# Optimization experiments

Measured on AMD Instinct MI355X. Metric: run time of the kernel, lower is better.

Reference implementation:

```python
import jax, jax.numpy as jnp
import numpy as np
import math

C = 512
D = C // 4  # 128
SCALE = math.sqrt(D)

def setup_inputs() -> dict:
    key = jax.random.key(0)
    k1, k2, k3, k4 = jax.random.split(key, 4)
    x = jax.random.normal(k1, (8, C, 2048), dtype=jnp.float32)
    # q_conv and k_conv share the same weight (tied in the torch module)
    wqk = jax.random.normal(k2, (D, C), dtype=jnp.float32) * (1.0 / math.sqrt(C))
    wv = jax.random.normal(k3, (D, C), dtype=jnp.float32) * (1.0 / math.sqrt(C))
    bv = jax.random.normal(k4, (D,), dtype=jnp.float32) * 0.01
    return {"x": x, "wqk": wqk, "wv": wv, "bv": bv}

def reference(x, wqk, wv, bv):
    # x: [B, C, N]; 1x1 conv == matmul over channel dim
    xq = jnp.einsum('dc,bcn->bnd', wqk, x)          # [B, N, D]
    xk = jnp.einsum('dc,bcn->bdn', wqk, x)          # [B, D, N]
    xv = jnp.einsum('dc,bcn->bdn', wv, x) + bv[None, :, None]  # [B, D, N]
    energy = jnp.einsum('bnd,bdm->bnm', xq, xk) / SCALE  # [B, N, N]
    attention = jax.nn.softmax(energy, axis=-1)
    x_r = jnp.einsum('bdn,bnm->bdm', xv, attention)  # [B, D, N]
    return x_r
```

## Files before the change

### kernel.cpp

```cpp
#include <hip/hip_runtime.h>

typedef short short4v __attribute__((ext_vector_type(4)));
typedef short short8 __attribute__((ext_vector_type(8)));
typedef float floatx4 __attribute__((ext_vector_type(4)));
typedef unsigned int uint;
typedef unsigned short ushort;

#define CH 512
#define NN 2048
#define DD 128
#define RSCALE 0.08838834764831845f

__device__ __forceinline__ float bf2f(ushort u) {
    union { uint i; float f; } v; v.i = ((uint)u) << 16; return v.f;
}
__device__ __forceinline__ ushort f2bf(float f) {
    union { float f; uint u; } v; v.f = f;
    uint u = v.u;
    return (ushort)((u + 0x7fffu + ((u >> 16) & 1u)) >> 16);
}

__global__ __launch_bounds__(256) void k0_prep(
    const float* __restrict__ wqk, const float* __restrict__ wv,
    ushort* __restrict__ Wbf, float* __restrict__ lsum)
{
    int gid = blockIdx.x * 256 + threadIdx.x;
    int base = gid * 4;
    const float* src = (base < 65536) ? (wqk + base) : (wv + base - 65536);
    float4 v = *(const float4*)src;
    short4v o;
    o[0] = (short)f2bf(v.x); o[1] = (short)f2bf(v.y);
    o[2] = (short)f2bf(v.z); o[3] = (short)f2bf(v.w);
    *(short4v*)&Wbf[base] = o;
    if (gid < 16384) lsum[gid] = 0.0f;
}

__global__ __launch_bounds__(256) void k1_proj(
    const float* __restrict__ x,
    const ushort* __restrict__ Wbf,
    const float* __restrict__ bv,
    ushort* __restrict__ Q,
    ushort* __restrict__ VT)
{
    const int nt = blockIdx.x;
    const int b  = blockIdx.y;
    const int n0 = nt * 32;
    const int t = threadIdx.x;
    const int lane = t & 63, w = t >> 6, l15 = lane & 15, quad = lane >> 4;

    __shared__ __attribute__((aligned(16))) ushort As[32 * 40];
    __shared__ __attribute__((aligned(16))) ushort Bs[256 * 40];
    __shared__ __attribute__((aligned(16))) ushort Vt[128 * 40];

    floatx4 acc[2][4];
#pragma unroll
    for (int i = 0; i < 2; i++)
#pragma unroll
        for (int j = 0; j < 4; j++) acc[i][j] = (floatx4)(0.0f);

    const float* xb = x + b * (CH * NN) + n0;

    for (int c0 = 0; c0 < CH; c0 += 32) {
        {
            int n = t & 31, g = t >> 5;
            short4v v;
#pragma unroll
            for (int i = 0; i < 4; i++)
                v[i] = (short)f2bf(xb[(c0 + g * 4 + i) * NN + n]);
            *(short4v*)&As[n * 40 + g * 4] = v;
        }
#pragma unroll
        for (int rep = 0; rep < 4; rep++) {
            int idx = rep * 256 + t;
            int row = idx >> 2, g = idx & 3;
            *(short8*)&Bs[row * 40 + g * 8] = *(const short8*)&Wbf[row * CH + c0 + g * 8];
        }
        __syncthreads();
        short8 a0 = *(short8*)&As[(l15) * 40 + quad * 8];
        short8 a1 = *(short8*)&As[(16 + l15) * 40 + quad * 8];
#pragma unroll
        for (int dt2 = 0; dt2 < 4; dt2++) {
            short8 bf = *(short8*)&Bs[(w * 64 + dt2 * 16 + l15) * 40 + quad * 8];
            acc[0][dt2] = __builtin_amdgcn_mfma_f32_16x16x32_bf16(a0, bf, acc[0][dt2], 0, 0, 0);
            acc[1][dt2] = __builtin_amdgcn_mfma_f32_16x16x32_bf16(a1, bf, acc[1][dt2], 0, 0, 0);
        }
        __syncthreads();
    }

#pragma unroll
    for (int ns = 0; ns < 2; ns++)
#pragma unroll
        for (int dt2 = 0; dt2 < 4; dt2++) {
            int ds_ = w * 64 + dt2 * 16 + l15;
#pragma unroll
            for (int r = 0; r < 4; r++) {
                int nl = ns * 16 + quad * 4 + r;
                float val = acc[ns][dt2][r];
                if (ds_ < 128) {
                    Q[b * (NN * DD) + (n0 + nl) * DD + ds_] = f2bf(val);
                } else {
                    int dv = ds_ - 128;
                    Vt[dv * 40 + nl] = f2bf(val + bv[dv]);
                }
            }
        }
    __syncthreads();
#pragma unroll
    for (int rep = 0; rep < 2; rep++) {
        int idx = rep * 256 + t;
        int dv = idx >> 2, seg = idx & 3;
        *(short8*)&VT[((size_t)b * DD + dv) * NN + n0 + seg * 8] =
            *(short8*)&Vt[dv * 40 + seg * 8];
    }
}

__global__ __launch_bounds__(256) void kl_sum(
    const ushort* __restrict__ Q,
    float* __restrict__ lsum)
{
    int pid = blockIdx.x;
    const int b = blockIdx.y;
    int it = 0;
    while (pid >= (16 - it)) { pid -= (16 - it); it++; }
    const int jt = it + pid;
    const int i0 = it * 128, j0 = jt * 128;
    const int t = threadIdx.x;
    const int lane = t & 63, w = t >> 6, l15 = lane & 15, quad = lane >> 4;
    const int wi = (w >> 1) * 64, wj = (w & 1) * 64;

    __shared__ __attribute__((aligned(16))) ushort Qi[128 * 136];
    __shared__ __attribute__((aligned(16))) ushort Qj[128 * 136];

    const ushort* Qb = Q + b * (NN * DD);

#pragma unroll
    for (int rep = 0; rep < 8; rep++) {
        int idx = rep * 256 + t;
        int row = idx >> 4, g = idx & 15;
        *(short8*)&Qi[row * 136 + g * 8] = *(const short8*)&Qb[(i0 + row) * DD + g * 8];
        *(short8*)&Qj[row * 136 + g * 8] = *(const short8*)&Qb[(j0 + row) * DD + g * 8];
    }
    __syncthreads();

    floatx4 acc[4][4];
#pragma unroll
    for (int i = 0; i < 4; i++)
#pragma unroll
        for (int j = 0; j < 4; j++) acc[i][j] = (floatx4)(0.0f);

#pragma unroll
    for (int kd = 0; kd < 4; kd++) {
        short8 afr[4], bfr[4];
#pragma unroll
        for (int nt = 0; nt < 4; nt++)
            afr[nt] = *(short8*)&Qi[(wi + nt * 16 + l15) * 136 + kd * 32 + quad * 8];
#pragma unroll
        for (int mt = 0; mt < 4; mt++)
            bfr[mt] = *(short8*)&Qj[(wj + mt * 16 + l15) * 136 + kd * 32 + quad * 8];
#pragma unroll
        for (int nt = 0; nt < 4; nt++)
#pragma unroll
            for (int mt = 0; mt < 4; mt++)
                acc[nt][mt] = __builtin_amdgcn_mfma_f32_16x16x32_bf16(afr[nt], bfr[mt], acc[nt][mt], 0, 0, 0);
    }

    float cs[4] = {0.f, 0.f, 0.f, 0.f};
#pragma unroll
    for (int nt = 0; nt < 4; nt++) {
        float rs[4] = {0.f, 0.f, 0.f, 0.f};
#pragma unroll
        for (int mt = 0; mt < 4; mt++)
#pragma unroll
            for (int r = 0; r < 4; r++) {
                float p = __expf(acc[nt][mt][r] * RSCALE);
                rs[r] += p;
                cs[mt] += p;
            }
#pragma unroll
        for (int r = 0; r < 4; r++) {
            float s = rs[r];
            s += __shfl_xor(s, 1);
            s += __shfl_xor(s, 2);
            s += __shfl_xor(s, 4);
            s += __shfl_xor(s, 8);
            if (l15 == 0)
                atomicAdd(&lsum[b * NN + i0 + wi + nt * 16 + quad * 4 + r], s);
        }
    }
    if (it != jt) {
#pragma unroll
        for (int mt = 0; mt < 4; mt++) {
            float s = cs[mt];
            s += __shfl_xor(s, 16);
            s += __shfl_xor(s, 32);
            if (lane < 16)
                atomicAdd(&lsum[b * NN + j0 + wj + mt * 16 + l15], s);
        }
    }
}

__global__ __launch_bounds__(256) void k_fused(
    const ushort* __restrict__ Q,
    const ushort* __restrict__ VT,
    const float* __restrict__ lsum,
    float* __restrict__ part)
{
    const int mt = blockIdx.x;
    const int h  = blockIdx.y;
    const int b  = blockIdx.z;
    const int m0 = mt * 64;
    const int t = threadIdx.x;
    const int lane = t & 63, w = t >> 6, l15 = lane & 15, quad = lane >> 4;

    __shared__ __attribute__((aligned(16))) ushort Qm[64 * 136];
    __shared__ __attribute__((aligned(16))) ushort Qn[64 * 136];
    __shared__ __attribute__((aligned(16))) ushort Vs[128 * 72];
    __shared__ __attribute__((aligned(16))) ushort Ps[64 * 68];

    const ushort* Qb = Q + b * (NN * DD);
    const ushort* VTb = VT + (size_t)b * DD * NN;
    const float* lb = lsum + b * NN;

#pragma unroll
    for (int rep = 0; rep < 4; rep++) {
        int idx = rep * 256 + t;
        int row = idx >> 4, g = idx & 15;
        *(short8*)&Qm[row * 136 + g * 8] = *(const short8*)&Qb[(m0 + row) * DD + g * 8];
    }
    __syncthreads();

    short8 qm[4][4];
#pragma unroll
    for (int ms = 0; ms < 4; ms++)
#pragma unroll
        for (int kd = 0; kd < 4; kd++)
            qm[ms][kd] = *(short8*)&Qm[(ms * 16 + l15) * 136 + kd * 32 + quad * 8];

    floatx4 acc[2][4];
#pragma unroll
    for (int i = 0; i < 2; i++)
#pragma unroll
        for (int j = 0; j < 4; j++) acc[i][j] = (floatx4)(0.0f);

    const int nbeg = h * (NN / 2), nend = nbeg + (NN / 2);
    for (int n0c = nbeg; n0c < nend; n0c += 64) {
        float lw = lb[n0c + w * 16 + l15];
        __syncthreads();
#pragma unroll
        for (int rep = 0; rep < 4; rep++) {
            int idx = rep * 256 + t;
            int row = idx >> 4, g = idx & 15;
            *(short8*)&Qn[row * 136 + g * 8] = *(const short8*)&Qb[(n0c + row) * DD + g * 8];
        }
#pragma unroll
        for (int rep = 0; rep < 4; rep++) {
            int idx = rep * 256 + t;
            int d = idx >> 3, g = idx & 7;
            *(short8*)&Vs[d * 72 + g * 8] = *(const short8*)&VTb[(size_t)d * NN + n0c + g * 8];
        }
        __syncthreads();

        {
            float linv = 1.0f / lw;
            short8 bq[4];
#pragma unroll
            for (int kd = 0; kd < 4; kd++)
                bq[kd] = *(short8*)&Qn[(w * 16 + l15) * 136 + kd * 32 + quad * 8];
#pragma unroll
            for (int ms = 0; ms < 4; ms++) {
                floatx4 s = (floatx4)(0.0f);
#pragma unroll
                for (int kd = 0; kd < 4; kd++)
                    s = __builtin_amdgcn_mfma_f32_16x16x32_bf16(qm[ms][kd], bq[kd], s, 0, 0, 0);
#pragma unroll
                for (int r = 0; r < 4; r++) {
                    float p = __expf(s[r] * RSCALE) * linv;
                    Ps[(ms * 16 + quad * 4 + r) * 68 + w * 16 + l15] = f2bf(p);
                }
            }
        }
        __syncthreads();

#pragma unroll
        for (int kn = 0; kn < 2; kn++) {
            short8 va0 = *(short8*)&Vs[(w * 32 + l15) * 72 + kn * 32 + quad * 8];
            short8 va1 = *(short8*)&Vs[(w * 32 + 16 + l15) * 72 + kn * 32 + quad * 8];
#pragma unroll
            for (int mf = 0; mf < 4; mf++) {
                short8 pb = *(short8*)&Ps[(mf * 16 + l15) * 68 + kn * 32 + quad * 8];
                acc[0][mf] = __builtin_amdgcn_mfma_f32_16x16x32_bf16(va0, pb, acc[0][mf], 0, 0, 0);
                acc[1][mf] = __builtin_amdgcn_mfma_f32_16x16x32_bf16(va1, pb, acc[1][mf], 0, 0, 0);
            }
        }
    }

    float* ob = part + (size_t)h * (8 * DD * NN) + (size_t)b * DD * NN;
#pragma unroll
    for (int dsub = 0; dsub < 2; dsub++)
#pragma unroll
        for (int mf = 0; mf < 4; mf++)
#pragma unroll
            for (int r = 0; r < 4; r++) {
                int d = w * 32 + dsub * 16 + quad * 4 + r;
                ob[(size_t)d * NN + m0 + mf * 16 + l15] = acc[dsub][mf][r];
            }
}

__global__ __launch_bounds__(256) void k_reduce(
    const float* __restrict__ part, float* __restrict__ out)
{
    int gid = blockIdx.x * 256 + threadIdx.x;
    const size_t half = (size_t)8 * DD * NN;
    float4 a = *(const float4*)&part[gid * 4];
    float4 b = *(const float4*)&part[half + gid * 4];
    float4 o;
    o.x = a.x + b.x; o.y = a.y + b.y; o.z = a.z + b.z; o.w = a.w + b.w;
    *(float4*)&out[gid * 4] = o;
}

__global__ __launch_bounds__(256) void k1_fb(
    const float* __restrict__ x, const float* __restrict__ wqk,
    const float* __restrict__ wv, const float* __restrict__ bv,
    ushort* __restrict__ Q, ushort* __restrict__ V)
{
    const int nt = blockIdx.x;
    const int b  = blockIdx.y;
    const int n0 = nt * 32;
    const int t = threadIdx.x;
    const int lane = t & 63, w = t >> 6, l15 = lane & 15, quad = lane >> 4;

    __shared__ __attribute__((aligned(16))) ushort As[32 * 40];
    __shared__ __attribute__((aligned(16))) ushort Bs[256 * 40];

    floatx4 acc[2][4];
#pragma unroll
    for (int i = 0; i < 2; i++)
#pragma unroll
        for (int j = 0; j < 4; j++) acc[i][j] = (floatx4)(0.0f);

    const float* xb = x + b * (CH * NN) + n0;

    for (int c0 = 0; c0 < CH; c0 += 32) {
        {
            int n = t & 31, g = t >> 5;
            short4v v;
#pragma unroll
            for (int i = 0; i < 4; i++)
                v[i] = (short)f2bf(xb[(c0 + g * 4 + i) * NN + n]);
            *(short4v*)&As[n * 40 + g * 4] = v;
        }
#pragma unroll
        for (int rep = 0; rep < 16; rep++) {
            int idx = rep * 256 + t;
            int row = idx >> 4, cp = idx & 15;
            const float* wf = (row < 128) ? (wqk + row * CH) : (wv + (row - 128) * CH);
            uint pack = (uint)f2bf(wf[c0 + cp * 2]) | ((uint)f2bf(wf[c0 + cp * 2 + 1]) << 16);
            *(uint*)&Bs[row * 40 + cp * 2] = pack;
        }
        __syncthreads();
        short8 a0 = *(short8*)&As[(l15) * 40 + quad * 8];
        short8 a1 = *(short8*)&As[(16 + l15) * 40 + quad * 8];
#pragma unroll
        for (int dt2 = 0; dt2 < 4; dt2++) {
            short8 bf = *(short8*)&Bs[(w * 64 + dt2 * 16 + l15) * 40 + quad * 8];
            acc[0][dt2] = __builtin_amdgcn_mfma_f32_16x16x32_bf16(a0, bf, acc[0][dt2], 0, 0, 0);
            acc[1][dt2] = __builtin_amdgcn_mfma_f32_16x16x32_bf16(a1, bf, acc[1][dt2], 0, 0, 0);
        }
        __syncthreads();
    }
#pragma unroll
    for (int ns = 0; ns < 2; ns++)
#pragma unroll
        for (int dt2 = 0; dt2 < 4; dt2++) {
            int ds_ = w * 64 + dt2 * 16 + l15;
#pragma unroll
            for (int r = 0; r < 4; r++) {
                int n = n0 + ns * 16 + quad * 4 + r;
                float val = acc[ns][dt2][r];
                if (ds_ < 128) {
                    Q[b * (NN * DD) + n * DD + ds_] = f2bf(val);
                } else {
                    int dv = ds_ - 128;
                    V[b * (NN * DD) + n * DD + dv] = f2bf(val + bv[dv]);
                }
            }
        }
}

__global__ __launch_bounds__(256) void k2_norm(
    const ushort* __restrict__ Q, ushort* __restrict__ V)
{
    const int ntile = blockIdx.x;
    const int b = blockIdx.y;
    const int n0 = ntile * 64;
    const int t = threadIdx.x;
    const int lane = t & 63, w = t >> 6, l15 = lane & 15, quad = lane >> 4;

    __shared__ __attribute__((aligned(16))) ushort Qs[64 * 136];
    __shared__ __attribute__((aligned(16))) ushort Qm2[64 * 136];

    const ushort* Qb = Q + b * (NN * DD);

#pragma unroll
    for (int rep = 0; rep < 16; rep++) {
        int idx = rep * 256 + t;
        int row = idx >> 6, dp = idx & 63;
        *(uint*)&Qs[row * 136 + dp * 2] = *(const uint*)&Qb[(n0 + row) * DD + dp * 2];
    }
    __syncthreads();

    short8 afr[4];
#pragma unroll
    for (int kd = 0; kd < 4; kd++)
        afr[kd] = *(short8*)&Qs[(w * 16 + l15) * 136 + kd * 32 + quad * 8];

    float sums[4] = {0.f, 0.f, 0.f, 0.f};

    for (int m0 = 0; m0 < NN; m0 += 64) {
#pragma unroll
        for (int rep = 0; rep < 16; rep++) {
            int idx = rep * 256 + t;
            int row = idx >> 6, dp = idx & 63;
            *(uint*)&Qm2[row * 136 + dp * 2] = *(const uint*)&Qb[(m0 + row) * DD + dp * 2];
        }
        __syncthreads();
#pragma unroll
        for (int ct = 0; ct < 4; ct++) {
            floatx4 s = (floatx4)(0.0f);
#pragma unroll
            for (int kd = 0; kd < 4; kd++) {
                short8 bf = *(short8*)&Qm2[(ct * 16 + l15) * 136 + kd * 32 + quad * 8];
                s = __builtin_amdgcn_mfma_f32_16x16x32_bf16(afr[kd], bf, s, 0, 0, 0);
            }
#pragma unroll
            for (int r = 0; r < 4; r++)
                sums[r] += __expf(s[r] * RSCALE);
        }
        __syncthreads();
    }

#pragma unroll
    for (int r = 0; r < 4; r++) {
        float s = sums[r];
        s += __shfl_xor(s, 1);
        s += __shfl_xor(s, 2);
        s += __shfl_xor(s, 4);
        s += __shfl_xor(s, 8);
        sums[r] = s;
    }

    ushort* Vb = V + b * (NN * DD);
#pragma unroll
    for (int r = 0; r < 4; r++) {
        int n = n0 + w * 16 + quad * 4 + r;
        float inv = 1.0f / sums[r];
        short8 vv = *(short8*)&Vb[n * DD + l15 * 8];
        short8 o;
#pragma unroll
        for (int i = 0; i < 8; i++)
            o[i] = (short)f2bf(bf2f((ushort)vv[i]) * inv);
        *(short8*)&Vb[n * DD + l15 * 8] = o;
    }
}

__global__ __launch_bounds__(256) void k3_attn(
    const ushort* __restrict__ Q, const ushort* __restrict__ Vp,
    float* __restrict__ out)
{
    const int mtile = blockIdx.x;
    const int b = blockIdx.y;
    const int m0 = mtile * 64;
    const int t = threadIdx.x;
    const int lane = t & 63, w = t >> 6, l15 = lane & 15, quad = lane >> 4;

    __shared__ __attribute__((aligned(16))) ushort Qs[64 * 136];
    __shared__ __attribute__((aligned(16))) ushort Qn2[32 * 136];
    __shared__ __attribute__((aligned(16))) ushort Vs2[128 * 40];
    __shared__ __attribute__((aligned(16))) ushort Ps2[64 * 40];

    const ushort* Qb = Q + b * (NN * DD);
    const ushort* Vpb = Vp + b * (NN * DD);

#pragma unroll
    for (int rep = 0; rep < 16; rep++) {
        int idx = rep * 256 + t;
        int row = idx >> 6, dp = idx & 63;
        *(uint*)&Qs[row * 136 + dp * 2] = *(const uint*)&Qb[(m0 + row) * DD + dp * 2];
    }
    __syncthreads();

    short8 afr[4];
#pragma unroll
    for (int kd = 0; kd < 4; kd++)
        afr[kd] = *(short8*)&Qs[(w * 16 + l15) * 136 + kd * 32 + quad * 8];

    floatx4 acc[2][4];
#pragma unroll
    for (int s = 0; s < 2; s++)
#pragma unroll
        for (int mt = 0; mt < 4; mt++) acc[s][mt] = (floatx4)(0.0f);

    for (int n0c = 0; n0c < NN; n0c += 32) {
#pragma unroll
        for (int rep = 0; rep < 8; rep++) {
            int idx = rep * 256 + t;
            int row = idx >> 6, dp = idx & 63;
            *(uint*)&Qn2[row * 136 + dp * 2] = *(const uint*)&Qb[(n0c + row) * DD + dp * 2];
        }
#pragma unroll
        for (int rep = 0; rep < 8; rep++) {
            int idx = rep * 256 + t;
            int np = idx >> 7, d = idx & 127;
            uint v0 = Vpb[(n0c + np * 2) * DD + d];
            uint v1 = Vpb[(n0c + np * 2 + 1) * DD + d];
            *(uint*)&Vs2[d * 40 + np * 2] = v0 | (v1 << 16);
        }
        __syncthreads();

#pragma unroll
        for (int nt2 = 0; nt2 < 2; nt2++) {
            floatx4 s = (floatx4)(0.0f);
#pragma unroll
            for (int kd = 0; kd < 4; kd++) {
                short8 bf = *(short8*)&Qn2[(nt2 * 16 + l15) * 136 + kd * 32 + quad * 8];
                s = __builtin_amdgcn_mfma_f32_16x16x32_bf16(afr[kd], bf, s, 0, 0, 0);
            }
#pragma unroll
            for (int r = 0; r < 4; r++) {
                float p = __expf(s[r] * RSCALE);
                Ps2[(w * 16 + quad * 4 + r) * 40 + nt2 * 16 + l15] = f2bf(p);
            }
        }
        __syncthreads();

        short8 pb[4];
#pragma unroll
        for (int mt = 0; mt < 4; mt++)
            pb[mt] = *(short8*)&Ps2[(mt * 16 + l15) * 40 + quad * 8];
#pragma unroll
        for (int sub = 0; sub < 2; sub++) {
            short8 va = *(short8*)&Vs2[(w * 32 + sub * 16 + l15) * 40 + quad * 8];
#pragma unroll
            for (int mt = 0; mt < 4; mt++)
                acc[sub][mt] = __builtin_amdgcn_mfma_f32_16x16x32_bf16(va, pb[mt], acc[sub][mt], 0, 0, 0);
        }
        __syncthreads();
    }

    float* ob = out + (size_t)b * DD * NN;
#pragma unroll
    for (int sub = 0; sub < 2; sub++)
#pragma unroll
        for (int mt = 0; mt < 4; mt++)
#pragma unroll
            for (int r = 0; r < 4; r++) {
                int d = w * 32 + sub * 16 + quad * 4 + r;
                int m = m0 + mt * 16 + l15;
                ob[(size_t)d * NN + m] = acc[sub][mt][r];
            }
}

extern "C" void kernel_launch(void* const* d_in, const int* in_sizes, int n_in,
                              void* d_out, int out_size, void* d_ws, size_t ws_size,
                              hipStream_t stream) {
    const float* x   = (const float*)d_in[0];
    const float* wqk = (const float*)d_in[1];
    const float* wv  = (const float*)d_in[2];
    const float* bv  = (const float*)d_in[3];
    float* out = (float*)d_out;

    ushort* Q = (ushort*)d_ws;

    if (ws_size >= (size_t)33 * 1024 * 1024) {
        ushort* VT   = (ushort*)((char*)d_ws + (4u << 20));
        ushort* Wbf  = (ushort*)((char*)d_ws + (8u << 20));
        float*  lsum = (float*)((char*)d_ws + (8u << 20) + (256u << 10));
        float*  part = (float*)((char*)d_ws + (16u << 20));

        k0_prep<<<128, 256, 0, stream>>>(wqk, wv, Wbf, lsum);
        k1_proj<<<dim3(64, 8), 256, 0, stream>>>(x, Wbf, bv, Q, VT);
        kl_sum<<<dim3(136, 8), 256, 0, stream>>>(Q, lsum);
        k_fused<<<dim3(32, 2, 8), 256, 0, stream>>>(Q, VT, lsum, part);
        k_reduce<<<2048, 256, 0, stream>>>(part, out);
    } else {
        ushort* V = (ushort*)((char*)d_ws + (4u << 20));
        k1_fb<<<dim3(64, 8), 256, 0, stream>>>(x, wqk, wv, bv, Q, V);
        k2_norm<<<dim3(32, 8), 256, 0, stream>>>(Q, V);
        k3_attn<<<dim3(32, 8), 256, 0, stream>>>(Q, V, out);
    }
}
```

Measured before the change: 152.2 us.

## Replace split-K partial buffer and reduce kernel with atomic accumulation into output

The fused attention kernel now accumulates its two split halves straight into the output with float atomicAdd. The prep kernel zeroes the output first, which removes the separate reduce kernel and the 16 MB partial buffer round trip. The x-tile load in the projection kernel also changes from scalar strided loads to float4 loads along N, transposed into shared memory. Atomics add contention and make the summation order nondeterministic, and the scattered 2-byte LDS stores may cause bank conflicts.

```diff
diff --git a/kernel.cpp b/kernel.cpp
--- a/kernel.cpp
+++ b/kernel.cpp
@@ -22,16 +22,21 @@
 
 __global__ __launch_bounds__(256) void k0_prep(
     const float* __restrict__ wqk, const float* __restrict__ wv,
-    ushort* __restrict__ Wbf, float* __restrict__ lsum)
+    ushort* __restrict__ Wbf, float* __restrict__ lsum,
+    float* __restrict__ out)
 {
     int gid = blockIdx.x * 256 + threadIdx.x;
-    int base = gid * 4;
-    const float* src = (base < 65536) ? (wqk + base) : (wv + base - 65536);
-    float4 v = *(const float4*)src;
-    short4v o;
-    o[0] = (short)f2bf(v.x); o[1] = (short)f2bf(v.y);
-    o[2] = (short)f2bf(v.z); o[3] = (short)f2bf(v.w);
-    *(short4v*)&Wbf[base] = o;
+    float4 z; z.x = 0.f; z.y = 0.f; z.z = 0.f; z.w = 0.f;
+    *(float4*)&out[gid * 4] = z;
+    if (gid < 32768) {
+        int base = gid * 4;
+        const float* src = (base < 65536) ? (wqk + base) : (wv + base - 65536);
+        float4 v = *(const float4*)src;
+        short4v o;
+        o[0] = (short)f2bf(v.x); o[1] = (short)f2bf(v.y);
+        o[2] = (short)f2bf(v.z); o[3] = (short)f2bf(v.w);
+        *(short4v*)&Wbf[base] = o;
+    }
     if (gid < 16384) lsum[gid] = 0.0f;
 }
 
@@ -62,12 +67,13 @@
 
     for (int c0 = 0; c0 < CH; c0 += 32) {
         {
-            int n = t & 31, g = t >> 5;
-            short4v v;
-#pragma unroll
-            for (int i = 0; i < 4; i++)
-                v[i] = (short)f2bf(xb[(c0 + g * 4 + i) * NN + n]);
-            *(short4v*)&As[n * 40 + g * 4] = v;
+            int c  = t & 31;
+            int ng = t >> 5;
+            float4 v = *(const float4*)&xb[(c0 + c) * NN + ng * 4];
+            As[(ng * 4 + 0) * 40 + c] = f2bf(v.x);
+            As[(ng * 4 + 1) * 40 + c] = f2bf(v.y);
+            As[(ng * 4 + 2) * 40 + c] = f2bf(v.z);
+            As[(ng * 4 + 3) * 40 + c] = f2bf(v.w);
         }
 #pragma unroll
         for (int rep = 0; rep < 4; rep++) {
@@ -203,7 +209,7 @@
     const ushort* __restrict__ Q,
     const ushort* __restrict__ VT,
     const float* __restrict__ lsum,
-    float* __restrict__ part)
+    float* __restrict__ out)
 {
     const int mt = blockIdx.x;
     const int h  = blockIdx.y;
@@ -294,7 +300,7 @@
         }
     }
 
-    float* ob = part + (size_t)h * (8 * DD * NN) + (size_t)b * DD * NN;
+    float* ob = out + (size_t)b * DD * NN;
 #pragma unroll
     for (int dsub = 0; dsub < 2; dsub++)
 #pragma unroll
@@ -302,20 +308,8 @@
 #pragma unroll
             for (int r = 0; r < 4; r++) {
                 int d = w * 32 + dsub * 16 + quad * 4 + r;
-                ob[(size_t)d * NN + m0 + mf * 16 + l15] = acc[dsub][mf][r];
-            }
-}
-
-__global__ __launch_bounds__(256) void k_reduce(
-    const float* __restrict__ part, float* __restrict__ out)
-{
-    int gid = blockIdx.x * 256 + threadIdx.x;
-    const size_t half = (size_t)8 * DD * NN;
-    float4 a = *(const float4*)&part[gid * 4];
-    float4 b = *(const float4*)&part[half + gid * 4];
-    float4 o;
-    o.x = a.x + b.x; o.y = a.y + b.y; o.z = a.z + b.z; o.w = a.w + b.w;
-    *(float4*)&out[gid * 4] = o;
+                atomicAdd(&ob[(size_t)d * NN + m0 + mf * 16 + l15], acc[dsub][mf][r]);
+            }
 }
 
 __global__ __launch_bounds__(256) void k1_fb(
@@ -571,17 +565,15 @@
 
     ushort* Q = (ushort*)d_ws;
 
-    if (ws_size >= (size_t)33 * 1024 * 1024) {
+    if (ws_size >= (size_t)16 * 1024 * 1024) {
         ushort* VT   = (ushort*)((char*)d_ws + (4u << 20));
         ushort* Wbf  = (ushort*)((char*)d_ws + (8u << 20));
         float*  lsum = (float*)((char*)d_ws + (8u << 20) + (256u << 10));
-        float*  part = (float*)((char*)d_ws + (16u << 20));
-
-        k0_prep<<<128, 256, 0, stream>>>(wqk, wv, Wbf, lsum);
+
+        k0_prep<<<2048, 256, 0, stream>>>(wqk, wv, Wbf, lsum, out);
         k1_proj<<<dim3(64, 8), 256, 0, stream>>>(x, Wbf, bv, Q, VT);
         kl_sum<<<dim3(136, 8), 256, 0, stream>>>(Q, lsum);
-        k_fused<<<dim3(32, 2, 8), 256, 0, stream>>>(Q, VT, lsum, part);
-        k_reduce<<<2048, 256, 0, stream>>>(part, out);
+        k_fused<<<dim3(32, 2, 8), 256, 0, stream>>>(Q, VT, lsum, out);
     } else {
         ushort* V = (ushort*)((char*)d_ws + (4u << 20));
         k1_fb<<<dim3(64, 8), 256, 0, stream>>>(x, wqk, wv, bv, Q, V);
```

Result: no change. 152.5 us (+0.2%).
